# Optimization experiments

Hardware: AMD Instinct MI355X
Metric: run time of the kernel (lower is better)

Reference implementation:

```python
import jax, jax.numpy as jnp
import numpy as np

B, NQ, C = 4, 3136, 512
H_IMG, W_IMG = 56, 56
HEADS, D_MODEL, D_K, D_V = 8, 512, 512, 512
RATIO = 2
LN_EPS = 1e-3   # keras LayerNormalization default
BN_EPS = 1e-3   # keras BatchNormalization default


def setup_inputs() -> dict:
    key = jax.random.key(0)
    ks = jax.random.split(key, 16)
    s = 0.02
    inp = {
        'queries': jax.random.normal(ks[0], (B, NQ, C), jnp.float32),
        'keys': jax.random.normal(ks[1], (B, NQ, C), jnp.float32),
        'values': jax.random.normal(ks[2], (B, NQ, C), jnp.float32),
        'Wq': jax.random.normal(ks[3], (C, HEADS * D_K), jnp.float32) * s,
        'bq': jnp.zeros((HEADS * D_K,), jnp.float32),
        'Wk': jax.random.normal(ks[4], (C, HEADS * D_K), jnp.float32) * s,
        'bk': jnp.zeros((HEADS * D_K,), jnp.float32),
        'Wv': jax.random.normal(ks[5], (C, HEADS * D_V), jnp.float32) * s,
        'bv': jnp.zeros((HEADS * D_V,), jnp.float32),
        'Wo': jax.random.normal(ks[6], (HEADS * D_V, D_MODEL), jnp.float32) * s,
        'bo': jnp.zeros((D_MODEL,), jnp.float32),
        # depthwise conv: kernel (kh, kw, in_per_group=1, out=C)
        'sr_kernel': jax.random.normal(ks[7], (RATIO + 1, RATIO + 1, 1, C), jnp.float32) * s,
        'sr_bias': jnp.zeros((C,), jnp.float32),
        'ln_gamma': jnp.ones((C,), jnp.float32),
        'ln_beta': jnp.zeros((C,), jnp.float32),
        # 1x1 channels_first conv over the head axis of the score tensor
        'tw': jax.random.normal(ks[8], (HEADS, HEADS), jnp.float32) * s,
        'tb': jnp.zeros((HEADS,), jnp.float32),
        # BatchNormalization(axis=[0,1]) -> params per (batch, head)
        'bn_gamma': jnp.ones((B, HEADS), jnp.float32),
        'bn_beta': jnp.zeros((B, HEADS), jnp.float32),
    }
    return inp


def _forward(queries, keys, values, Wq, bq, Wk, bk, Wv, bv, Wo, bo,
             sr_kernel, sr_bias, ln_gamma, ln_beta, tw, tb, bn_gamma, bn_beta):
    b, nq, c = queries.shape
    # Q projection -> (b, h, nq, d_model)  (d_k == d_model)
    q = (queries @ Wq + bq).reshape(b, nq, HEADS, D_MODEL).transpose(0, 2, 1, 3)
    # spatial reduction of K/V source (ratio > 1 path; keys/values args unused)
    x = queries.reshape(b, H_IMG, W_IMG, c)
    x = jax.lax.conv_general_dilated(
        x, sr_kernel, window_strides=(RATIO, RATIO), padding='SAME',
        dimension_numbers=('NHWC', 'HWIO', 'NHWC'), feature_group_count=c) + sr_bias
    x = x.reshape(b, -1, c)  # (b, nk, c), nk = (H/ratio)*(W/ratio)
    mu = jnp.mean(x, axis=-1, keepdims=True)
    var = jnp.mean(jnp.square(x - mu), axis=-1, keepdims=True)
    x = (x - mu) * jax.lax.rsqrt(var + LN_EPS) * ln_gamma + ln_beta
    k = (x @ Wk + bk).reshape(b, -1, HEADS, D_MODEL).transpose(0, 2, 1, 3)
    v = (x @ Wv + bv).reshape(b, -1, HEADS, D_MODEL).transpose(0, 2, 1, 3)
    # scores (b, h, nq, nk)
    att = jnp.einsum('bhqd,bhkd->bhqk', q, k) / np.sqrt(D_K).astype(np.float32)
    # transform: 1x1 conv over head channel, softmax over k, BN over (q, k)
    att = jnp.einsum('bhqk,hg->bgqk', att, tw) + tb[:, None, None]
    att = jax.nn.softmax(att, axis=-1)
    m = jnp.mean(att, axis=(2, 3), keepdims=True)
    s2 = jnp.mean(jnp.square(att - m), axis=(2, 3), keepdims=True)
    att = bn_gamma[:, :, None, None] * (att - m) * jax.lax.rsqrt(s2 + BN_EPS) \
          + bn_beta[:, :, None, None]
    # attend and project out
    out = jnp.einsum('bhqk,bhkd->bhqd', att, v)
    out = out.transpose(0, 2, 1, 3).reshape(b, nq, HEADS * D_V)
    return out @ Wo + bo


def reference(queries, keys, values, Wq, bq, Wk, bk, Wv, bv, Wo, bo,
              sr_kernel, sr_bias, ln_gamma, ln_beta, tw, tb, bn_gamma, bn_beta):
    return _forward(queries, keys, values, Wq, bq, Wk, bk, Wv, bv, Wo, bo,
                    sr_kernel, sr_bias, ln_gamma, ln_beta, tw, tb, bn_gamma, bn_beta)
```

## Files before the change

### kernel.cpp

```cpp
#include <hip/hip_runtime.h>
#include <hip/hip_bf16.h>
#include <math.h>

typedef unsigned short u16;
typedef __attribute__((ext_vector_type(4))) float f32x4;
typedef __attribute__((ext_vector_type(8))) __bf16 bf16x8;

#define B_    4
#define NQ_   3136
#define C_    512
#define HIMG  56
#define WIMG  56
#define HD_   4096
#define NK_   784
#define NKP_  832

static __device__ __forceinline__ float b2f(u16 u){
  union { unsigned int i; float f; } v; v.i = ((unsigned int)u)<<16; return v.f;
}
static __device__ __forceinline__ u16 f2b(float f){
  union { float f; unsigned int i; } v; v.f = f;
  unsigned int r = v.i + 0x7fffu + ((v.i>>16)&1u);
  return (u16)(r>>16);
}

#define GLD16(gsrc, ldst) __builtin_amdgcn_global_load_lds( \
    (const __attribute__((address_space(1))) void*)(gsrc), \
    (__attribute__((address_space(3))) void*)(ldst), 16, 0, 0)

static __device__ __forceinline__ void xcd_order(int &bx, int &by, int &bz){
  const int nx = gridDim.x, ny = gridDim.y, nz = gridDim.z;
  long l = blockIdx.x + (long)nx*(blockIdx.y + (long)ny*blockIdx.z);
  const long n = (long)nx*ny*nz;
  long g = ((n&7)==0) ? ((l&7)*(n>>3) + (l>>3)) : l;
  bx = (int)(g % nx); g /= nx;
  by = (int)(g % ny);
  bz = (int)(g / ny);
}

template<int OUT_F32>
__global__ __launch_bounds__(256, 2)
void gemm128(const u16* __restrict__ A, const u16* __restrict__ Bm, void* __restrict__ Cm,
             int M, int Ncols, int K, int sA, int sB, int sC, int zdiv,
             long long zA1, long long zA2, long long zB1, long long zB2,
             long long zC1, long long zC2,
             const float* __restrict__ bias1, float hscale,
             const float* __restrict__ scalePtr,
             const float* __restrict__ bias2, int rowsPerB, int b2s)
{
  __shared__ u16 lds[36864];
  int bx, by, z;
  xcd_order(bx, by, z);
  const int zq = z / zdiv, zr = z % zdiv;
  const u16* Ab = A  + (long long)zq*zA1 + (long long)zr*zA2;
  const u16* Bb = Bm + (long long)zq*zB1 + (long long)zr*zB2;
  const int m0 = bx*256, n0 = by*128;
  const int t = threadIdx.x, w = t>>6, lane = t&63;
  const int wm = w>>1, wn = w&1;
  const int l15 = lane & 15;

  const int srow = t>>2;
  const int scol = (((t&3) ^ ((srow>>1)&3)) << 3);
  const u16* aS = Ab + (long long)(m0 + srow)*sA + scol;
  const u16* bS = Bb + (long long)(n0 + srow)*sB + scol;
  const long long sA64 = (long long)64*sA, sB64 = (long long)64*sB;
  const int w512 = w*512;

#define STAGE(jt, buf) do{                                        \
    const u16* a0_ = aS + (long long)(jt)*32;                     \
    const u16* b0_ = bS + (long long)(jt)*32;                     \
    u16* la_ = lds + (buf)*8192 + w512;                           \
    u16* lb_ = lds + 24576 + (buf)*4096 + w512;                   \
    GLD16(a0_,          la_);                                     \
    GLD16(a0_ +   sA64, la_ + 2048);                              \
    GLD16(a0_ + 2*sA64, la_ + 4096);                              \
    GLD16(a0_ + 3*sA64, la_ + 6144);                              \
    GLD16(b0_,          lb_);                                     \
    GLD16(b0_ +   sB64, lb_ + 2048);                              \
  }while(0)

  f32x4 acc[8][4];
#pragma unroll
  for(int i=0;i<8;i++)
#pragma unroll
    for(int j=0;j<4;j++) acc[i][j] = (f32x4)(0.0f);

  const char* ldsc = (const char*)lds;
  const int ck = (((lane>>4) ^ ((lane>>1)&3)) << 4);
  const int aRowB = (wm*128 + l15) * 64;
  const int bRowB = (wn*64  + l15) * 64;

  const int T = K >> 5;
  STAGE(0, 0);
  STAGE(1, 1);

  int buf = 0;
  for(int j=0; j<T; j++){
    if(j == T-1) asm volatile("s_waitcnt vmcnt(0)" ::: "memory");
    else         asm volatile("s_waitcnt vmcnt(6)" ::: "memory");
    asm volatile("s_barrier" ::: "memory");

    const int aBuf = buf*16384 + aRowB;
    const int bBuf = 49152 + buf*8192 + bRowB;
    bf16x8 af[8], bfv[4];
#pragma unroll
    for(int fr=0; fr<8; fr++) af[fr]  = *(const bf16x8*)(ldsc + aBuf + fr*1024 + ck);
#pragma unroll
    for(int fn=0; fn<4; fn++) bfv[fn] = *(const bf16x8*)(ldsc + bBuf + fn*1024 + ck);
    {
      const int nbuf = (buf+2 >= 3) ? buf-1 : buf+2;
      if(j+2 < T) STAGE(j+2, nbuf);
    }
    __builtin_amdgcn_s_setprio(1);
#pragma unroll
    for(int fr=0; fr<8; fr++)
#pragma unroll
      for(int fn=0; fn<4; fn++)
        acc[fr][fn] = __builtin_amdgcn_mfma_f32_16x16x32_bf16(af[fr], bfv[fn], acc[fr][fn], 0,0,0);
    __builtin_amdgcn_s_setprio(0);
    buf = (buf+1 >= 3) ? 0 : buf+1;
  }
#undef STAGE

  const float dsc = scalePtr ? scalePtr[z] : 1.0f;
  const long long cBase = (long long)zq*zC1 + (long long)zr*zC2;
  const int r4 = (lane>>4)*4;
#pragma unroll
  for(int mf=0; mf<8; mf++){
    const int row0 = m0 + wm*128 + mf*16 + r4;
#pragma unroll
    for(int nf=0; nf<4; nf++){
      const int col = n0 + wn*64 + nf*16 + l15;
      if(col < Ncols){
#pragma unroll
        for(int r=0;r<4;r++){
          const int row = row0 + r;
          if(row < M){
            float v = acc[mf][nf][r];
            if(bias1) v += bias1[col];
            v *= hscale * dsc;
            if(bias2) v += bias2[(row/rowsPerB)*b2s + col];
            if(OUT_F32) ((float*)Cm)[cBase + (long long)row*sC + col] = v;
            else        ((u16*) Cm)[cBase + (long long)row*sC + col] = f2b(v);
          }
        }
      }
    }
  }
}

__global__ __launch_bounds__(256)
void wt_kernel(const float* __restrict__ W, u16* __restrict__ Wt, int K, int N){
  __shared__ float tile[32][33];
  const int n0 = blockIdx.x*32, k0 = blockIdx.y*32;
  const int t = threadIdx.x, tr = t>>5, tc = t&31;
#pragma unroll
  for(int i=0;i<4;i++)
    tile[tr+i*8][tc] = W[(long long)(k0+tr+i*8)*N + n0+tc];
  __syncthreads();
#pragma unroll
  for(int i=0;i<4;i++)
    Wt[(long long)(n0+tr+i*8)*K + k0+tc] = f2b(tile[tc][tr+i*8]);
}

__global__ __launch_bounds__(256)
void cvt_bf16(const float* __restrict__ in, u16* __restrict__ outp, long long n){
  long long i = ((long long)blockIdx.x*256 + threadIdx.x)*4;
  if(i+3 < n){
    float4 v = *(const float4*)(in+i);
    ushort4 o; o.x=f2b(v.x); o.y=f2b(v.y); o.z=f2b(v.z); o.w=f2b(v.w);
    *(ushort4*)(outp+i) = o;
  }
}

__global__ __launch_bounds__(256)
void conv_ln(const float* __restrict__ q, const float* __restrict__ ker,
             const float* __restrict__ cbias, const float* __restrict__ gamma,
             const float* __restrict__ beta, u16* __restrict__ xo)
{
  const int p = blockIdx.x;
  const int b = p / 784, pix = p % 784;
  const int oy = pix / 28, ox = pix % 28;
  const int t = threadIdx.x;
  __shared__ float red[256];
  float v[2];
#pragma unroll
  for(int e=0;e<2;e++){
    const int c = t + e*256;
    float acc = cbias[c];
    for(int ky=0;ky<3;ky++){
      const int y = oy*2 + ky;
      if(y >= HIMG) continue;
      for(int kx=0;kx<3;kx++){
        const int x = ox*2 + kx;
        if(x >= WIMG) continue;
        acc += q[(((long long)b*HIMG + y)*WIMG + x)*C_ + c] * ker[(ky*3+kx)*C_ + c];
      }
    }
    v[e] = acc;
  }
  red[t]=v[0]+v[1]; __syncthreads();
  for(int st=128; st>0; st>>=1){ if(t<st) red[t]+=red[t+st]; __syncthreads(); }
  const float mu = red[0] * (1.0f/C_);
  __syncthreads();
  const float d0=v[0]-mu, d1=v[1]-mu;
  red[t]=d0*d0+d1*d1; __syncthreads();
  for(int st=128; st>0; st>>=1){ if(t<st) red[t]+=red[t+st]; __syncthreads(); }
  const float rs = rsqrtf(red[0]*(1.0f/C_) + 1e-3f);
  const long long ob = (long long)p*C_;
#pragma unroll
  for(int e=0;e<2;e++){
    const int c = t+e*256;
    xo[ob+c] = f2b((v[e]-mu)*rs*gamma[c] + beta[c]);
  }
}

__global__ __launch_bounds__(256)
void vt_kernel(const u16* __restrict__ Vf_b, u16* __restrict__ Vt_b, int sV){
  __shared__ u16 tile[32][33];
  const int k0 = blockIdx.x*32, d0 = blockIdx.y*32;
  const int t = threadIdx.x, tr = t>>5, tc = t&31;
#pragma unroll
  for(int i=0;i<4;i++){
    const int k = k0+tr+i*8;
    tile[tr+i*8][tc] = (k < NK_) ? Vf_b[(long long)k*sV + d0+tc] : (u16)0;
  }
  __syncthreads();
#pragma unroll
  for(int i=0;i<4;i++)
    Vt_b[(long long)(d0+tr+i*8)*NKP_ + k0+tc] = tile[tc][tr+i*8];
}

__global__ __launch_bounds__(512)
void mix_softmax(u16* __restrict__ S_b, const float* __restrict__ tw,
                 float* __restrict__ partial_b)
{
  const int qi = blockIdx.x;
  const int t = threadIdx.x;
  const int wave = t >> 6, lane = t & 63;
  __shared__ float sv[8*NK_];
  const long long rowstr = (long long)NQ_*NKP_;
  const long long base = (long long)qi*NKP_;

  for(int idx = t; idx < 8*196; idx += 512){
    const int h = idx / 196, c4 = idx % 196;
    ushort4 u4 = *(const ushort4*)(S_b + base + h*rowstr + c4*4);
    float* d = sv + h*NK_ + c4*4;
    d[0]=b2f(u4.x); d[1]=b2f(u4.y); d[2]=b2f(u4.z); d[3]=b2f(u4.w);
  }
  __syncthreads();

  const int g = wave;
  float wgt[8];
#pragma unroll
  for(int h=0;h<8;h++) wgt[h] = tw[h*8+g];

  float xs[13];
  float lmax = -1e30f;
#pragma unroll
  for(int j=0;j<13;j++){
    const int k = j*64 + lane;
    if(k < NK_){
      float x = 0.f;
#pragma unroll
      for(int h=0;h<8;h++) x += wgt[h]*sv[h*NK_+k];
      xs[j] = x;
      lmax = fmaxf(lmax, x);
    } else xs[j] = -1e30f;
  }
#pragma unroll
  for(int off=32; off>=1; off>>=1) lmax = fmaxf(lmax, __shfl_xor(lmax, off));

  float lsum = 0.f;
#pragma unroll
  for(int j=0;j<13;j++){
    const int k = j*64 + lane;
    if(k < NK_){
      const float e = __expf(xs[j] - lmax);
      xs[j] = e; lsum += e;
    }
  }
#pragma unroll
  for(int off=32; off>=1; off>>=1) lsum += __shfl_xor(lsum, off);
  const float inv = 1.0f/lsum;

  u16* dst = S_b + base + g*rowstr;
  float lss = 0.f;
#pragma unroll
  for(int j=0;j<13;j++){
    const int k = j*64 + lane;
    if(k < NK_){
      const float dev = xs[j]*inv - (1.0f/NK_);
      dst[k] = f2b(dev);
      lss += dev*dev;
    }
  }
  for(int k = NK_ + lane; k < NKP_; k += 64) dst[k] = 0;
#pragma unroll
  for(int off=32; off>=1; off>>=1) lss += __shfl_xor(lss, off);
  if(lane==0) partial_b[g*NQ_ + qi] = lss;
}

__global__ __launch_bounds__(256)
void colsum_v(const u16* __restrict__ Vf_b, float* __restrict__ part, int sV){
  const int hd = blockIdx.x*256 + threadIdx.x;
  const int kc = blockIdx.y;
  const u16* p = Vf_b + (long long)kc*98*sV + hd;
  float s=0.f;
  for(int k=0;k<98;k++) s += b2f(p[(long long)k*sV]);
  part[(long long)kc*HD_ + hd] = s;
}

__global__ __launch_bounds__(256)
void finalize_stats(const float* __restrict__ partial_b, const float* __restrict__ bng_b,
                    const float* __restrict__ bnb_b, float* __restrict__ a_b,
                    float* __restrict__ c_b){
  const int g = blockIdx.x;
  const int t = threadIdx.x;
  __shared__ float red[4];
  float s = 0.f;
  for(int i=t; i<NQ_; i+=256) s += partial_b[g*NQ_ + i];
#pragma unroll
  for(int off=32; off>=1; off>>=1) s += __shfl_xor(s, off);
  if((t&63)==0) red[t>>6] = s;
  __syncthreads();
  if(t==0){
    const float tot = red[0]+red[1]+red[2]+red[3];
    const float s2 = tot * (1.0f/((float)NQ_*(float)NK_));
    a_b[g] = bng_b[g]*rsqrtf(s2 + 1e-3f);
    c_b[g] = bnb_b[g];
  }
}

__global__ __launch_bounds__(256)
void corr_kernel(const float* __restrict__ part, const u16* __restrict__ Wot,
                 const float* __restrict__ c_b, float* __restrict__ corr_b){
  const int n = blockIdx.x, t = threadIdx.x;
  __shared__ float red[256];
  float s = 0.f;
  for(int hd=t; hd<HD_; hd+=256){
    float cs = 0.f;
#pragma unroll
    for(int kc=0; kc<8; kc++) cs += part[(long long)kc*HD_ + hd];
    s += c_b[hd>>9] * cs * b2f(Wot[(long long)n*HD_+hd]);
  }
  red[t]=s; __syncthreads();
  for(int st=128; st>0; st>>=1){ if(t<st) red[t]+=red[t+st]; __syncthreads(); }
  if(t==0) corr_b[n]=red[0];
}

extern "C" void kernel_launch(void* const* d_in, const int* in_sizes, int n_in,
                              void* d_out, int out_size, void* d_ws, size_t ws_size,
                              hipStream_t stream)
{
  (void)in_sizes; (void)n_in; (void)out_size;
  const float* queries = (const float*)d_in[0];
  const float* Wq  = (const float*)d_in[3];
  const float* bq  = (const float*)d_in[4];
  const float* Wk  = (const float*)d_in[5];
  const float* bk  = (const float*)d_in[6];
  const float* Wv  = (const float*)d_in[7];
  const float* bv  = (const float*)d_in[8];
  const float* Wo  = (const float*)d_in[9];
  const float* bo  = (const float*)d_in[10];
  const float* srk = (const float*)d_in[11];
  const float* srb = (const float*)d_in[12];
  const float* lng = (const float*)d_in[13];
  const float* lnb = (const float*)d_in[14];
  const float* tw  = (const float*)d_in[15];
  const float* bng = (const float*)d_in[17];
  const float* bnb = (const float*)d_in[18];
  float* out = (float*)d_out;
  const float QSC = 0.04419417382415922f;

  char* w = (char*)d_ws;
  size_t off = 0;
  auto alloc = [&](size_t bytes)->char*{
    char* p = w + off; off += (bytes + 255) & ~(size_t)255; return p;
  };

  const bool tierA = (ws_size >= (size_t)210*1024*1024);

  u16* Wqt = (u16*)alloc((size_t)HD_*C_*2);
  u16* Wkt = (u16*)alloc((size_t)HD_*C_*2);
  u16* Wvt = (u16*)alloc((size_t)HD_*C_*2);
  u16* Wot = (u16*)alloc((size_t)C_*HD_*2);
  u16* x   = (u16*)alloc((size_t)B_*NK_*C_*2 + 262144);
  float* bkv = (float*)alloc((size_t)2*HD_*4);
  u16* Qin;
  u16* QfU;
  if(tierA){
    Qin = (u16*)alloc((size_t)B_*NQ_*C_*2);
    QfU = (u16*)alloc((size_t)B_*NQ_*HD_*2 + 2097152);
  } else {
    Qin = (u16*)alloc((size_t)NQ_*C_*2 + 262144);
    QfU = (u16*)alloc((size_t)NQ_*HD_*2 + 2097152);
  }
  u16* KV_b = (u16*)alloc((size_t)NK_*2*HD_*2 + 4194304);
  u16* Vt_b = (u16*)alloc((size_t)HD_*NKP_*2);
  u16* S_b  = (u16*)alloc((size_t)8*NQ_*NKP_*2 + 524288);
  float* colsum  = (float*)alloc((size_t)8*HD_*4);
  float* partial = (float*)alloc((size_t)8*NQ_*4);
  float* aArr    = (float*)alloc(256);
  float* cArr    = (float*)alloc(256);
  float* corrB   = (float*)alloc((size_t)B_*C_*4);

  wt_kernel<<<dim3(128,16), 256, 0, stream>>>(Wq, Wqt, 512, 4096);
  wt_kernel<<<dim3(128,16), 256, 0, stream>>>(Wk, Wkt, 512, 4096);
  wt_kernel<<<dim3(128,16), 256, 0, stream>>>(Wv, Wvt, 512, 4096);
  wt_kernel<<<dim3(16,128), 256, 0, stream>>>(Wo, Wot, 4096, 512);
  conv_ln<<<B_*NK_, 256, 0, stream>>>(queries, srk, srb, lng, lnb, x);
  hipMemcpyAsync(bkv,      bk, HD_*4, hipMemcpyDeviceToDevice, stream);
  hipMemcpyAsync(bkv+HD_,  bv, HD_*4, hipMemcpyDeviceToDevice, stream);

  if(tierA){
    cvt_bf16<<<6272, 256, 0, stream>>>(queries, Qin, (long long)B_*NQ_*C_);
    gemm128<0><<<dim3(49,32,1),256,0,stream>>>(Qin, Wqt, QfU, B_*NQ_, 4096, 512,
        512, 512, HD_, 1, 0,0,0,0,0,0, bq, QSC, nullptr, nullptr, 1, 0);
  }

  for(int b=0; b<B_; b++){
    u16* Qf_b = tierA ? (QfU + (size_t)b*NQ_*HD_) : QfU;
    if(!tierA){
      cvt_bf16<<<1568, 256, 0, stream>>>(queries + (size_t)b*NQ_*C_, Qin, (long long)NQ_*C_);
      gemm128<0><<<dim3(13,32,1),256,0,stream>>>(Qin, Wqt, Qf_b, NQ_, 4096, 512,
          512, 512, HD_, 1, 0,0,0,0,0,0, bq, QSC, nullptr, nullptr, 1, 0);
    }
    const u16* x_b = x + (size_t)b*NK_*C_;
    gemm128<0><<<dim3(4,64,1),256,0,stream>>>(x_b, Wkt, KV_b, NK_, 2*HD_, 512,
        512, 512, 2*HD_, 1, 0,0,0,0,0,0, bkv, 1.0f, nullptr, nullptr, 1, 0);
    vt_kernel<<<dim3(26,128),256,0,stream>>>(KV_b + HD_, Vt_b, 2*HD_);
    colsum_v<<<dim3(16,8),256,0,stream>>>(KV_b + HD_, colsum, 2*HD_);
    gemm128<0><<<dim3(13,7,8),256,0,stream>>>(Qf_b, KV_b, S_b, NQ_, NKP_, 512,
        HD_, 2*HD_, NKP_, 8, 0, 512, 0, 512, 0, (long long)NQ_*NKP_,
        nullptr, 1.0f, nullptr, nullptr, 1, 0);
    mix_softmax<<<NQ_, 512, 0, stream>>>(S_b, tw, partial);
    finalize_stats<<<8,256,0,stream>>>(partial, bng + b*8, bnb + b*8, aArr + b*8, cArr + b*8);
    corr_kernel<<<512,256,0,stream>>>(colsum, Wot, cArr + b*8, corrB + b*C_);
    gemm128<0><<<dim3(13,4,8),256,0,stream>>>(S_b, Vt_b, Qf_b, NQ_, 512, NKP_,
        NKP_, NKP_, HD_, 8, 0, (long long)NQ_*NKP_, 0, (long long)512*NKP_, 0, 512,
        nullptr, 1.0f, aArr + b*8, nullptr, 1, 0);
    if(!tierA){
      gemm128<1><<<dim3(13,4,1),256,0,stream>>>(Qf_b, Wot, out + (size_t)b*NQ_*C_,
          NQ_, 512, HD_, HD_, HD_, C_,
          1, 0,0,0,0,0,0, bo, 1.0f, nullptr, corrB + b*C_, NQ_, C_);
    }
  }

  if(tierA){
    gemm128<1><<<dim3(49,4,1),256,0,stream>>>(QfU, Wot, out, B_*NQ_, 512, HD_,
        HD_, HD_, C_, 1, 0,0,0,0,0,0, bo, 1.0f, nullptr, corrB, NQ_, C_);
  }
}
```

Before: 938.9 us.

## Fold Q and K projections into per-head Gram matrix, drop Q projection GEMM

Replaces the explicit Q projection (4096-wide) and K projection with a precomputed per-head 512x512 matrix G_h = Wq_h·Wk_h^T, so scores become queries·(x·G_h)^T plus a bias term computed from bq. V is produced directly transposed by a GEMM with Wv, and the column-sum correction is derived algebraically from colsum(x)·Wv plus the bias. The score layout changes to an interleaved per-query slab, and block ordering now balances tiles across XCDs. This removes the large Q GEMM and the V transpose at the cost of extra small kernels, and it adds bf16 rounding of the fused G matrix.

After: 969.9 us. +3.3%, slower.

```diff
diff --git a/kernel.cpp b/kernel.cpp
--- a/kernel.cpp
+++ b/kernel.cpp
@@ -13,7 +13,8 @@
 #define WIMG  56
 #define HD_   4096
 #define NK_   784
-#define NKP_  832
+#define SLAB  800
+#define SROW  6400
 
 static __device__ __forceinline__ float b2f(u16 u){
   union { unsigned int i; float f; } v; v.i = ((unsigned int)u)<<16; return v.f;
@@ -28,14 +29,16 @@
     (const __attribute__((address_space(1))) void*)(gsrc), \
     (__attribute__((address_space(3))) void*)(ldst), 16, 0, 0)
 
-static __device__ __forceinline__ void xcd_order(int &bx, int &by, int &bz){
+static __device__ __forceinline__ void order_byinner(int &bx, int &by, int &bz){
   const int nx = gridDim.x, ny = gridDim.y, nz = gridDim.z;
-  long l = blockIdx.x + (long)nx*(blockIdx.y + (long)ny*blockIdx.z);
+  const long l = blockIdx.x + (long)nx*(blockIdx.y + (long)ny*blockIdx.z);
   const long n = (long)nx*ny*nz;
-  long g = ((n&7)==0) ? ((l&7)*(n>>3) + (l>>3)) : l;
-  bx = (int)(g % nx); g /= nx;
-  by = (int)(g % ny);
-  bz = (int)(g / ny);
+  const long q8 = n>>3, r8 = n&7;
+  const long xcd = l&7, idx = l>>3;
+  long g = (xcd<r8 ? xcd*(q8+1) : r8*(q8+1) + (xcd-r8)*q8) + idx;
+  by = (int)(g % ny); g /= ny;
+  bx = (int)(g % nx);
+  bz = (int)(g / nx);
 }
 
 template<int OUT_F32>
@@ -50,7 +53,7 @@
 {
   __shared__ u16 lds[36864];
   int bx, by, z;
-  xcd_order(bx, by, z);
+  order_byinner(bx, by, z);
   const int zq = z / zdiv, zr = z % zdiv;
   const u16* Ab = A  + (long long)zq*zA1 + (long long)zr*zA2;
   const u16* Bb = Bm + (long long)zq*zB1 + (long long)zr*zB2;
@@ -216,37 +219,60 @@
 }
 
 __global__ __launch_bounds__(256)
-void vt_kernel(const u16* __restrict__ Vf_b, u16* __restrict__ Vt_b, int sV){
-  __shared__ u16 tile[32][33];
-  const int k0 = blockIdx.x*32, d0 = blockIdx.y*32;
-  const int t = threadIdx.x, tr = t>>5, tc = t&31;
-#pragma unroll
-  for(int i=0;i<4;i++){
-    const int k = k0+tr+i*8;
-    tile[tr+i*8][tc] = (k < NK_) ? Vf_b[(long long)k*sV + d0+tc] : (u16)0;
-  }
-  __syncthreads();
-#pragma unroll
-  for(int i=0;i<4;i++)
-    Vt_b[(long long)(d0+tr+i*8)*NKP_ + k0+tc] = tile[tc][tr+i*8];
+void u_kernel(const float* __restrict__ Wk, const float* __restrict__ bq,
+              float* __restrict__ u, float qsc){
+  const int id = blockIdx.x*256 + threadIdx.x;
+  const int h = id >> 9, c = id & 511;
+  float s = 0.f;
+  for(int e=0; e<512; e++) s += Wk[(long long)c*HD_ + h*512 + e] * bq[h*512 + e];
+  u[id] = s * qsc;
+}
+
+__global__ __launch_bounds__(256)
+void r_kernel(const u16* __restrict__ x_b, const float* __restrict__ u,
+              float* __restrict__ r_b){
+  const int id = blockIdx.x*256 + threadIdx.x;
+  if(id >= 8*NK_) return;
+  const int h = id / NK_, k = id % NK_;
+  float s = 0.f;
+  for(int c=0; c<512; c++) s += u[h*512+c] * b2f(x_b[(long long)k*512 + c]);
+  r_b[id] = s;
+}
+
+__global__ __launch_bounds__(256)
+void cx_kernel(const u16* __restrict__ x_b, float* __restrict__ cx){
+  const int c = blockIdx.x*256 + threadIdx.x;
+  float s = 0.f;
+  for(int k=0; k<NK_; k++) s += b2f(x_b[(long long)k*512 + c]);
+  cx[c] = s;
+}
+
+__global__ __launch_bounds__(256)
+void vv_kernel(const float* __restrict__ cx, const float* __restrict__ Wv,
+               float* __restrict__ vv){
+  const int e = blockIdx.x*256 + threadIdx.x;
+  float s = 0.f;
+  for(int c=0; c<512; c++) s += cx[c] * Wv[(long long)c*HD_ + e];
+  vv[e] = s;
 }
 
 __global__ __launch_bounds__(512)
 void mix_softmax(u16* __restrict__ S_b, const float* __restrict__ tw,
-                 float* __restrict__ partial_b)
+                 const float* __restrict__ r_b, float* __restrict__ partial_b)
 {
   const int qi = blockIdx.x;
   const int t = threadIdx.x;
   const int wave = t >> 6, lane = t & 63;
   __shared__ float sv[8*NK_];
-  const long long rowstr = (long long)NQ_*NKP_;
-  const long long base = (long long)qi*NKP_;
+  const long long base = (long long)qi*SROW;
 
   for(int idx = t; idx < 8*196; idx += 512){
     const int h = idx / 196, c4 = idx % 196;
-    ushort4 u4 = *(const ushort4*)(S_b + base + h*rowstr + c4*4);
+    ushort4 u4 = *(const ushort4*)(S_b + base + h*SLAB + c4*4);
+    float4 rv = *(const float4*)(r_b + h*NK_ + c4*4);
     float* d = sv + h*NK_ + c4*4;
-    d[0]=b2f(u4.x); d[1]=b2f(u4.y); d[2]=b2f(u4.z); d[3]=b2f(u4.w);
+    d[0]=b2f(u4.x)+rv.x; d[1]=b2f(u4.y)+rv.y;
+    d[2]=b2f(u4.z)+rv.z; d[3]=b2f(u4.w)+rv.w;
   }
   __syncthreads();
 
@@ -284,7 +310,7 @@
   for(int off=32; off>=1; off>>=1) lsum += __shfl_xor(lsum, off);
   const float inv = 1.0f/lsum;
 
-  u16* dst = S_b + base + g*rowstr;
+  u16* dst = S_b + base + g*SLAB;
   float lss = 0.f;
 #pragma unroll
   for(int j=0;j<13;j++){
@@ -295,20 +321,10 @@
       lss += dev*dev;
     }
   }
-  for(int k = NK_ + lane; k < NKP_; k += 64) dst[k] = 0;
+  if(lane < 16) dst[NK_ + lane] = 0;
 #pragma unroll
   for(int off=32; off>=1; off>>=1) lss += __shfl_xor(lss, off);
   if(lane==0) partial_b[g*NQ_ + qi] = lss;
-}
-
-__global__ __launch_bounds__(256)
-void colsum_v(const u16* __restrict__ Vf_b, float* __restrict__ part, int sV){
-  const int hd = blockIdx.x*256 + threadIdx.x;
-  const int kc = blockIdx.y;
-  const u16* p = Vf_b + (long long)kc*98*sV + hd;
-  float s=0.f;
-  for(int k=0;k<98;k++) s += b2f(p[(long long)k*sV]);
-  part[(long long)kc*HD_ + hd] = s;
 }
 
 __global__ __launch_bounds__(256)
@@ -333,17 +349,14 @@
 }
 
 __global__ __launch_bounds__(256)
-void corr_kernel(const float* __restrict__ part, const u16* __restrict__ Wot,
-                 const float* __restrict__ c_b, float* __restrict__ corr_b){
+void corr_kernel(const float* __restrict__ vv, const float* __restrict__ bv,
+                 const u16* __restrict__ Wot, const float* __restrict__ c_b,
+                 float* __restrict__ corr_b){
   const int n = blockIdx.x, t = threadIdx.x;
   __shared__ float red[256];
   float s = 0.f;
-  for(int hd=t; hd<HD_; hd+=256){
-    float cs = 0.f;
-#pragma unroll
-    for(int kc=0; kc<8; kc++) cs += part[(long long)kc*HD_ + hd];
-    s += c_b[hd>>9] * cs * b2f(Wot[(long long)n*HD_+hd]);
-  }
+  for(int e=t; e<HD_; e+=256)
+    s += c_b[e>>9] * (vv[e] + 784.0f*bv[e]) * b2f(Wot[(long long)n*HD_+e]);
   red[t]=s; __syncthreads();
   for(int st=128; st>0; st>>=1){ if(t<st) red[t]+=red[t+st]; __syncthreads(); }
   if(t==0) corr_b[n]=red[0];
@@ -353,12 +366,11 @@
                               void* d_out, int out_size, void* d_ws, size_t ws_size,
                               hipStream_t stream)
 {
-  (void)in_sizes; (void)n_in; (void)out_size;
+  (void)in_sizes; (void)n_in; (void)out_size; (void)ws_size;
   const float* queries = (const float*)d_in[0];
   const float* Wq  = (const float*)d_in[3];
   const float* bq  = (const float*)d_in[4];
   const float* Wk  = (const float*)d_in[5];
-  const float* bk  = (const float*)d_in[6];
   const float* Wv  = (const float*)d_in[7];
   const float* bv  = (const float*)d_in[8];
   const float* Wo  = (const float*)d_in[9];
@@ -379,76 +391,63 @@
     char* p = w + off; off += (bytes + 255) & ~(size_t)255; return p;
   };
 
-  const bool tierA = (ws_size >= (size_t)210*1024*1024);
-
-  u16* Wqt = (u16*)alloc((size_t)HD_*C_*2);
-  u16* Wkt = (u16*)alloc((size_t)HD_*C_*2);
   u16* Wvt = (u16*)alloc((size_t)HD_*C_*2);
   u16* Wot = (u16*)alloc((size_t)C_*HD_*2);
+  u16* Gt  = (u16*)alloc((size_t)8*C_*C_*2 + 262144);
   u16* x   = (u16*)alloc((size_t)B_*NK_*C_*2 + 262144);
-  float* bkv = (float*)alloc((size_t)2*HD_*4);
-  u16* Qin;
-  u16* QfU;
-  if(tierA){
-    Qin = (u16*)alloc((size_t)B_*NQ_*C_*2);
-    QfU = (u16*)alloc((size_t)B_*NQ_*HD_*2 + 2097152);
-  } else {
-    Qin = (u16*)alloc((size_t)NQ_*C_*2 + 262144);
-    QfU = (u16*)alloc((size_t)NQ_*HD_*2 + 2097152);
-  }
-  u16* KV_b = (u16*)alloc((size_t)NK_*2*HD_*2 + 4194304);
-  u16* Vt_b = (u16*)alloc((size_t)HD_*NKP_*2);
-  u16* S_b  = (u16*)alloc((size_t)8*NQ_*NKP_*2 + 524288);
-  float* colsum  = (float*)alloc((size_t)8*HD_*4);
+  u16* Qin = (u16*)alloc((size_t)B_*NQ_*C_*2 + 262144);
+  u16* U   = (u16*)alloc((size_t)B_*NQ_*HD_*2);
+  char* scratch = alloc((size_t)56262656);
+  u16* Wkc = (u16*)scratch;
+  u16* Wqc = (u16*)(scratch + 4194304);
+  u16* S_b  = (u16*)scratch;
+  u16* Vt_b = (u16*)(scratch + 42762240);
+  u16* H_b  = (u16*)(scratch + 49577984);
+  float* uArr    = (float*)alloc((size_t)HD_*4);
+  float* rArr    = (float*)alloc((size_t)8*NK_*4);
+  float* cx      = (float*)alloc((size_t)C_*4);
+  float* vv      = (float*)alloc((size_t)HD_*4);
   float* partial = (float*)alloc((size_t)8*NQ_*4);
   float* aArr    = (float*)alloc(256);
   float* cArr    = (float*)alloc(256);
   float* corrB   = (float*)alloc((size_t)B_*C_*4);
 
-  wt_kernel<<<dim3(128,16), 256, 0, stream>>>(Wq, Wqt, 512, 4096);
-  wt_kernel<<<dim3(128,16), 256, 0, stream>>>(Wk, Wkt, 512, 4096);
   wt_kernel<<<dim3(128,16), 256, 0, stream>>>(Wv, Wvt, 512, 4096);
   wt_kernel<<<dim3(16,128), 256, 0, stream>>>(Wo, Wot, 4096, 512);
+  cvt_bf16<<<2048, 256, 0, stream>>>(Wk, Wkc, (long long)C_*HD_);
+  cvt_bf16<<<2048, 256, 0, stream>>>(Wq, Wqc, (long long)C_*HD_);
+  cvt_bf16<<<6272, 256, 0, stream>>>(queries, Qin, (long long)B_*NQ_*C_);
   conv_ln<<<B_*NK_, 256, 0, stream>>>(queries, srk, srb, lng, lnb, x);
-  hipMemcpyAsync(bkv,      bk, HD_*4, hipMemcpyDeviceToDevice, stream);
-  hipMemcpyAsync(bkv+HD_,  bv, HD_*4, hipMemcpyDeviceToDevice, stream);
-
-  if(tierA){
-    cvt_bf16<<<6272, 256, 0, stream>>>(queries, Qin, (long long)B_*NQ_*C_);
-    gemm128<0><<<dim3(49,32,1),256,0,stream>>>(Qin, Wqt, QfU, B_*NQ_, 4096, 512,
-        512, 512, HD_, 1, 0,0,0,0,0,0, bq, QSC, nullptr, nullptr, 1, 0);
-  }
+  u_kernel<<<16, 256, 0, stream>>>(Wk, bq, uArr, QSC);
+
+  gemm128<0><<<dim3(2,4,8),256,0,stream>>>(Wqc, Wkc, Gt, 512, 512, 512,
+      HD_, HD_, 512, 8, 0, 512, 0, 512, 0, (long long)C_*C_,
+      nullptr, QSC, nullptr, nullptr, 1, 0);
 
   for(int b=0; b<B_; b++){
-    u16* Qf_b = tierA ? (QfU + (size_t)b*NQ_*HD_) : QfU;
-    if(!tierA){
-      cvt_bf16<<<1568, 256, 0, stream>>>(queries + (size_t)b*NQ_*C_, Qin, (long long)NQ_*C_);
-      gemm128<0><<<dim3(13,32,1),256,0,stream>>>(Qin, Wqt, Qf_b, NQ_, 4096, 512,
-          512, 512, HD_, 1, 0,0,0,0,0,0, bq, QSC, nullptr, nullptr, 1, 0);
-    }
     const u16* x_b = x + (size_t)b*NK_*C_;
-    gemm128<0><<<dim3(4,64,1),256,0,stream>>>(x_b, Wkt, KV_b, NK_, 2*HD_, 512,
-        512, 512, 2*HD_, 1, 0,0,0,0,0,0, bkv, 1.0f, nullptr, nullptr, 1, 0);
-    vt_kernel<<<dim3(26,128),256,0,stream>>>(KV_b + HD_, Vt_b, 2*HD_);
-    colsum_v<<<dim3(16,8),256,0,stream>>>(KV_b + HD_, colsum, 2*HD_);
-    gemm128<0><<<dim3(13,7,8),256,0,stream>>>(Qf_b, KV_b, S_b, NQ_, NKP_, 512,
-        HD_, 2*HD_, NKP_, 8, 0, 512, 0, 512, 0, (long long)NQ_*NKP_,
+    const u16* Qin_b = Qin + (size_t)b*NQ_*C_;
+    u16* U_b = U + (size_t)b*NQ_*HD_;
+
+    gemm128<0><<<dim3(4,4,8),256,0,stream>>>(x_b, Gt, H_b, NK_, 512, 512,
+        512, 512, 512, 8, 0, 0, 0, (long long)C_*C_, 0, (long long)NK_*512,
         nullptr, 1.0f, nullptr, nullptr, 1, 0);
-    mix_softmax<<<NQ_, 512, 0, stream>>>(S_b, tw, partial);
+    r_kernel<<<25, 256, 0, stream>>>(x_b, uArr, rArr);
+    gemm128<0><<<dim3(13,7,8),256,0,stream>>>(Qin_b, H_b, S_b, NQ_, NK_, 512,
+        512, 512, SROW, 8, 0, 0, 0, (long long)NK_*512, 0, SLAB,
+        nullptr, 1.0f, nullptr, nullptr, 1, 0);
+    gemm128<0><<<dim3(16,7,1),256,0,stream>>>(Wvt, x_b, Vt_b, HD_, NK_, 512,
+        512, 512, SLAB, 1, 0,0,0,0,0,0, nullptr, 1.0f, nullptr, nullptr, 1, 0);
+    cx_kernel<<<2, 256, 0, stream>>>(x_b, cx);
+    vv_kernel<<<16, 256, 0, stream>>>(cx, Wv, vv);
+    mix_softmax<<<NQ_, 512, 0, stream>>>(S_b, tw, rArr, partial);
     finalize_stats<<<8,256,0,stream>>>(partial, bng + b*8, bnb + b*8, aArr + b*8, cArr + b*8);
-    corr_kernel<<<512,256,0,stream>>>(colsum, Wot, cArr + b*8, corrB + b*C_);
-    gemm128<0><<<dim3(13,4,8),256,0,stream>>>(S_b, Vt_b, Qf_b, NQ_, 512, NKP_,
-        NKP_, NKP_, HD_, 8, 0, (long long)NQ_*NKP_, 0, (long long)512*NKP_, 0, 512,
+    corr_kernel<<<512,256,0,stream>>>(vv, bv, Wot, cArr + b*8, corrB + b*C_);
+    gemm128<0><<<dim3(13,4,8),256,0,stream>>>(S_b, Vt_b, U_b, NQ_, 512, SLAB,
+        SROW, SLAB, HD_, 8, 0, SLAB, 0, (long long)512*SLAB, 0, 512,
         nullptr, 1.0f, aArr + b*8, nullptr, 1, 0);
-    if(!tierA){
-      gemm128<1><<<dim3(13,4,1),256,0,stream>>>(Qf_b, Wot, out + (size_t)b*NQ_*C_,
-          NQ_, 512, HD_, HD_, HD_, C_,
-          1, 0,0,0,0,0,0, bo, 1.0f, nullptr, corrB + b*C_, NQ_, C_);
-    }
-  }
-
-  if(tierA){
-    gemm128<1><<<dim3(49,4,1),256,0,stream>>>(QfU, Wot, out, B_*NQ_, 512, HD_,
-        HD_, HD_, C_, 1, 0,0,0,0,0,0, bo, 1.0f, nullptr, corrB, NQ_, C_);
-  }
-}
+  }
+
+  gemm128<1><<<dim3(49,4,1),256,0,stream>>>(U, Wot, out, B_*NQ_, 512, HD_,
+      HD_, HD_, C_, 1, 0,0,0,0,0,0, bo, 1.0f, nullptr, corrB, NQ_, C_);
+}
```
